# Kernel optimization log

Hardware: AMD Instinct MI355X
Metric: run time of the kernel (lower is better)

The kernel has to match this reference:

```python
import math
import jax, jax.numpy as jnp
import numpy as np


def get_slopes(n):
    def pow2(n):
        start = 2.0 ** (-(2.0 ** (-(math.log2(n) - 3))))
        return [start * (start ** i) for i in range(n)]
    if math.log2(n).is_integer():
        return pow2(n)
    c = 2 ** math.floor(math.log2(n))
    return pow2(c) + get_slopes(2 * c)[0::2][: n - c]


def setup_inputs() -> dict:
    key = jax.random.key(0)
    B, T, C = 2, 2048, 1024
    ks = jax.random.split(key, 9)
    std = 0.02
    n_layers = 12
    inp = {
        "x": jax.random.normal(ks[0], (B, T, C), dtype=jnp.float32),
        # weights stored as [in, out] (transpose of torch Linear.weight)
        "Wq": std * jax.random.normal(ks[1], (C, C), dtype=jnp.float32),
        "bq": jnp.zeros((C,), dtype=jnp.float32),
        "Wk": std * jax.random.normal(ks[2], (C, C), dtype=jnp.float32),
        "bk": jnp.zeros((C,), dtype=jnp.float32),
        "Wv": std * jax.random.normal(ks[3], (C, C), dtype=jnp.float32),
        "bv": jnp.zeros((C,), dtype=jnp.float32),
        # fc_resid gets std 0.02/sqrt(2*num_layers)
        "Wo": (std / math.sqrt(2 * n_layers)) * jax.random.normal(ks[4], (C, C), dtype=jnp.float32),
        "bo": jnp.zeros((C,), dtype=jnp.float32),
        "n_head": 16,
    }
    return inp


def reference(x, Wq, bq, Wk, bk, Wv, bv, Wo, bo, n_head):
    B, T, C = x.shape
    hd = C // n_head
    # QKV projections, split heads: [B, nh, T, hd]
    def proj(W, b):
        return (x @ W + b).reshape(B, T, n_head, hd).transpose(0, 2, 1, 3)
    q, k, v = proj(Wq, bq), proj(Wk, bk), proj(Wv, bv)

    # ALiBi bias: bias[h, i, j] = -slope_h * (i - j) for j <= i, -inf above diag
    slopes = jnp.asarray(get_slopes(n_head), dtype=x.dtype)  # [nh]
    idx = jnp.arange(T)
    dist = (idx[:, None] - idx[None, :]).astype(x.dtype)  # [T, T], i - j
    bias = -slopes[:, None, None] * dist  # [nh, T, T]
    causal = idx[:, None] >= idx[None, :]
    bias = jnp.where(causal[None], bias, jnp.asarray(-jnp.inf, dtype=x.dtype))

    scale = 1.0 / math.sqrt(hd)
    scores = jnp.einsum("bnqh,bnkh->bnqk", q, k) * scale + bias[None]
    att = jax.nn.softmax(scores, axis=-1)
    y = jnp.einsum("bnqk,bnkh->bnqh", att, v)  # [B, nh, T, hd]
    y = y.transpose(0, 2, 1, 3).reshape(B, T, C)
    return y @ Wo + bo
```

## Files before the change

kernel.cpp:

```cpp
#include <hip/hip_runtime.h>


typedef unsigned short u16;
typedef unsigned int u32;
typedef __attribute__((ext_vector_type(8))) short bf16x8;
typedef __attribute__((ext_vector_type(4))) float f32x4;
typedef __attribute__((ext_vector_type(4))) unsigned short u16x4;

#define MFMA16x16(A, B, C_) __builtin_amdgcn_mfma_f32_16x16x32_bf16((A), (B), (C_), 0, 0, 0)

__device__ __forceinline__ u16 f2bf(float f) {
  u32 x = __builtin_bit_cast(u32, f);
  x += 0x7fff + ((x >> 16) & 1);
  return (u16)(x >> 16);
}

__device__ __forceinline__ void gload_lds16(const u16* g, u16* l) {
  __builtin_amdgcn_global_load_lds(
      (const __attribute__((address_space(1))) void*)g,
      (__attribute__((address_space(3))) void*)l, 16, 0, 0);
}

constexpr int T = 2048, C = 1024, HD = 64;
constexpr int BT = 2 * T;

__device__ __forceinline__ bf16x8 ldsfrag(const u16* lds, int row, int kchunk) {
  return *(const bf16x8*)(lds + row * 64 + (((kchunk) ^ (row & 7)) << 3));
}

__global__ __launch_bounds__(256) void convert_x_kernel(
    const float* __restrict__ xin, u16* __restrict__ xc) {
  int i = (blockIdx.x * 256 + threadIdx.x) * 8;
  const float4 a = *(const float4*)(xin + i);
  const float4 b = *(const float4*)(xin + i + 4);
  uint4 o;
  o.x = (u32)f2bf(a.x) | ((u32)f2bf(a.y) << 16);
  o.y = (u32)f2bf(a.z) | ((u32)f2bf(a.w) << 16);
  o.z = (u32)f2bf(b.x) | ((u32)f2bf(b.y) << 16);
  o.w = (u32)f2bf(b.z) | ((u32)f2bf(b.w) << 16);
  *(uint4*)(xc + i) = o;
}

__global__ __launch_bounds__(256) void transpose4_kernel(
    const float* __restrict__ w0, const float* __restrict__ w1,
    const float* __restrict__ w2, const float* __restrict__ w3,
    u16* __restrict__ wqkvT, u16* __restrict__ woT) {
  __shared__ u16 tile[32][33];
  const int z = blockIdx.z;
  const float* in = (z == 0) ? w0 : (z == 1) ? w1 : (z == 2) ? w2 : w3;
  u16* out = (z < 3) ? (wqkvT + (size_t)z * (1u << 20)) : woT;
  int tx = threadIdx.x, ty = threadIdx.y;
  int x = blockIdx.x * 32 + tx;
#pragma unroll
  for (int i = 0; i < 4; i++) {
    int y = blockIdx.y * 32 + ty + i * 8;
    tile[ty + i * 8][tx] = f2bf(in[y * 1024 + x]);
  }
  __syncthreads();
  int xo = blockIdx.y * 32 + tx;
#pragma unroll
  for (int i = 0; i < 4; i++) {
    int yo = blockIdx.x * 32 + ty + i * 8;
    out[yo * 1024 + xo] = tile[tx][ty + i * 8];
  }
}

__global__ __launch_bounds__(256) void gemm_qkv_kernel(
    const u16* __restrict__ A, const u16* __restrict__ Bt,
    const float* __restrict__ b0, const float* __restrict__ b1,
    const float* __restrict__ b2,
    u16* __restrict__ qout, u16* __restrict__ kout, u16* __restrict__ vtout) {
  constexpr int K = 1024;
  __shared__ __align__(16) u16 As[128 * 64];
  __shared__ __align__(16) u16 Bs[128 * 64];

  const int tid = threadIdx.x;
  const int w = tid >> 6, lane = tid & 63;
  const int l15 = lane & 15, quad = lane >> 4;
  const int m0 = blockIdx.y * 128, n0 = blockIdx.x * 128;
  const int wm = (w >> 1) * 64, wn = (w & 1) * 64;
  const int gsub = (lane & 7) ^ ((lane >> 3) & 7);
  const int rsub = lane >> 3;

  f32x4 acc[4][4] = {};
  const u16* Ag = A + (size_t)m0 * K;
  const u16* Bg = Bt + (size_t)n0 * K;

  for (int k0 = 0; k0 < K; k0 += 64) {
    __syncthreads();
#pragma unroll
    for (int t = 0; t < 4; t++) {
      int rbase = w * 32 + t * 8;
      gload_lds16(Ag + (size_t)(rbase + rsub) * K + k0 + gsub * 8, As + rbase * 64);
      gload_lds16(Bg + (size_t)(rbase + rsub) * K + k0 + gsub * 8, Bs + rbase * 64);
    }
    __syncthreads();
#pragma unroll
    for (int ks = 0; ks < 2; ks++) {
      bf16x8 af[4], bf[4];
#pragma unroll
      for (int mi = 0; mi < 4; mi++)
        af[mi] = ldsfrag(As, wm + mi * 16 + l15, (ks << 2) | quad);
#pragma unroll
      for (int ni = 0; ni < 4; ni++)
        bf[ni] = ldsfrag(Bs, wn + ni * 16 + l15, (ks << 2) | quad);
#pragma unroll
      for (int mi = 0; mi < 4; mi++)
#pragma unroll
        for (int ni = 0; ni < 4; ni++)
          acc[mi][ni] = MFMA16x16(af[mi], bf[ni], acc[mi][ni]);
    }
  }

  const int sel = n0 >> 10;
  const int nloc = n0 & 1023;
  if (sel < 2) {
    u16* D = (sel == 0) ? qout : kout;
    const float* bias = (sel == 0) ? b0 : b1;
#pragma unroll
    for (int mi = 0; mi < 4; mi++)
#pragma unroll
      for (int ni = 0; ni < 4; ni++) {
        int rb = m0 + wm + mi * 16 + quad * 4;
        int col = nloc + wn + ni * 16 + l15;
        float bb = bias[col];
#pragma unroll
        for (int r = 0; r < 4; r++)
          D[(size_t)(rb + r) * 1024 + col] = f2bf(acc[mi][ni][r] + bb);
      }
  } else {
#pragma unroll
    for (int mi = 0; mi < 4; mi++)
#pragma unroll
      for (int ni = 0; ni < 4; ni++) {
        int rb = m0 + wm + mi * 16 + quad * 4;
        int c = nloc + wn + ni * 16 + l15;
        float bb = b2[c];
        u16x4 pk;
#pragma unroll
        for (int r = 0; r < 4; r++) pk[r] = f2bf(acc[mi][ni][r] + bb);
        *(u16x4*)(vtout + (size_t)c * 4096 + rb) = pk;
      }
  }
}

__global__ __launch_bounds__(256) void gemm_out_kernel(
    const u16* __restrict__ A, const u16* __restrict__ Bt,
    const float* __restrict__ bias, float* __restrict__ fout) {
  constexpr int K = 1024;
  __shared__ __align__(16) u16 As[128 * 64];
  __shared__ __align__(16) u16 Bs[64 * 64];

  const int tid = threadIdx.x;
  const int w = tid >> 6, lane = tid & 63;
  const int l15 = lane & 15, quad = lane >> 4;
  const int m0 = blockIdx.y * 128, n0 = blockIdx.x * 64;
  const int wm = (w >> 1) * 64, wn = (w & 1) * 32;
  const int gsub = (lane & 7) ^ ((lane >> 3) & 7);
  const int rsub = lane >> 3;

  f32x4 acc[4][2] = {};
  const u16* Ag = A + (size_t)m0 * K;
  const u16* Bg = Bt + (size_t)n0 * K;

  for (int k0 = 0; k0 < K; k0 += 64) {
    __syncthreads();
#pragma unroll
    for (int t = 0; t < 4; t++) {
      int rbase = w * 32 + t * 8;
      gload_lds16(Ag + (size_t)(rbase + rsub) * K + k0 + gsub * 8, As + rbase * 64);
    }
#pragma unroll
    for (int t = 0; t < 2; t++) {
      int rbase = w * 16 + t * 8;
      gload_lds16(Bg + (size_t)(rbase + rsub) * K + k0 + gsub * 8, Bs + rbase * 64);
    }
    __syncthreads();
#pragma unroll
    for (int ks = 0; ks < 2; ks++) {
      bf16x8 af[4], bf[2];
#pragma unroll
      for (int mi = 0; mi < 4; mi++)
        af[mi] = ldsfrag(As, wm + mi * 16 + l15, (ks << 2) | quad);
#pragma unroll
      for (int ni = 0; ni < 2; ni++)
        bf[ni] = ldsfrag(Bs, wn + ni * 16 + l15, (ks << 2) | quad);
#pragma unroll
      for (int mi = 0; mi < 4; mi++)
#pragma unroll
        for (int ni = 0; ni < 2; ni++)
          acc[mi][ni] = MFMA16x16(af[mi], bf[ni], acc[mi][ni]);
    }
  }

#pragma unroll
  for (int mi = 0; mi < 4; mi++)
#pragma unroll
    for (int ni = 0; ni < 2; ni++) {
      int rb = m0 + wm + mi * 16 + quad * 4;
      int col = n0 + wn + ni * 16 + l15;
      float bb = bias[col];
#pragma unroll
      for (int r = 0; r < 4; r++)
        fout[(size_t)(rb + r) * 1024 + col] = acc[mi][ni][r] + bb;
    }
}

__global__ __launch_bounds__(512, 4) void attn_kernel(
    const u16* __restrict__ qbuf, const u16* __restrict__ kbuf,
    const u16* __restrict__ vtbuf, u16* __restrict__ ybuf) {
  __shared__ __align__(16) u16 Qs[64 * 64];
  __shared__ __align__(16) u16 KVs[4][64 * 64];
  __shared__ __align__(16) u16 Ps[8][16 * 64];

  const int tid = threadIdx.x;
  const int w = tid >> 6, lane = tid & 63;
  const int wq = w & 3, g = w >> 2;
  const int l15 = lane & 15, quad = lane >> 4;
  const int bh = blockIdx.y, b = bh >> 4, h = bh & 15;
  const float slope = exp2f(-0.5f * (float)(h + 1));
  const float slope128 = slope * 128.f;
  const int gsub = (lane & 7) ^ ((lane >> 3) & 7);
  const int rsub = lane >> 3;

  const u16* kbase0 = kbuf + (size_t)b * T * C + h * HD;
  const u16* vtbase0 = vtbuf + (size_t)h * HD * BT + (size_t)b * T;
  u16* Pw = Ps[w];
  const int st = w >> 1;
  const int skind = st & 1;
  const int sjt = st >> 1;
  const int srb = (w & 1) * 32;

#pragma unroll 1
  for (int half = 0; half < 2; half++) {
    const int qt = half == 0 ? (31 - (int)blockIdx.x) : (int)blockIdx.x;

    __syncthreads();
    const u16* qb = qbuf + (size_t)(b * T + qt * 64) * C + h * HD;
    gload_lds16(qb + (size_t)(w * 8 + rsub) * C + gsub * 8, Qs + (w * 8) * 64);
    __syncthreads();
    bf16x8 aq0 = ldsfrag(Qs, wq * 16 + l15, quad);
    bf16x8 aq1 = ldsfrag(Qs, wq * 16 + l15, 4 + quad);

    f32x4 o[4] = {};
    float lsum[4] = {0.f, 0.f, 0.f, 0.f};
    float br[4][4];
    const int ig0 = qt * 64 + wq * 16 + quad * 4;
#pragma unroll
    for (int ni = 0; ni < 4; ni++)
#pragma unroll
      for (int r = 0; r < 4; r++)
        br[ni][r] = slope * (float)(g * 64 + ni * 16 + l15 - ig0 - r);

    const int iters = (qt + 2) >> 1;
#pragma unroll 1
    for (int it = 0; it < iters; it++) {
      __syncthreads();
      {
        int jtv = 2 * it + sjt;
        int jtr = jtv > qt ? qt : jtv;
        const u16* base = skind ? (vtbase0 + jtr * 64)
                                : (kbase0 + (size_t)jtr * 64 * C);
        const int stride = skind ? BT : C;
        u16* dst = KVs[skind * 2 + sjt] + srb * 64;
#pragma unroll
        for (int c2 = 0; c2 < 4; c2++)
          gload_lds16(base + (size_t)(srb + c2 * 8 + rsub) * stride + gsub * 8,
                      dst + c2 * 8 * 64);
      }
      __syncthreads();

      const int jtv = 2 * it + g;
      const u16* Kw = KVs[g];
      const u16* Vw = KVs[2 + g];

      f32x4 s[4];
#pragma unroll
      for (int ni = 0; ni < 4; ni++) {
        bf16x8 kf0 = ldsfrag(Kw, ni * 16 + l15, quad);
        bf16x8 kf1 = ldsfrag(Kw, ni * 16 + l15, 4 + quad);
        f32x4 z = {0.f, 0.f, 0.f, 0.f};
        z = MFMA16x16(aq0, kf0, z);
        z = MFMA16x16(aq1, kf1, z);
        s[ni] = z;
      }

      const bool edge = (jtv >= qt);
#pragma unroll
      for (int ni = 0; ni < 4; ni++)
#pragma unroll
        for (int r = 0; r < 4; r++) {
          float p = __expf(fmaf(s[ni][r], 0.125f, br[ni][r]));
          if (edge && (jtv * 64 + ni * 16 + l15) > (ig0 + r)) p = 0.f;
          lsum[r] += p;
          int prow = quad * 4 + r, pcol = ni * 16 + l15;
          Pw[prow * 64 + (((pcol >> 3) ^ (prow & 7)) << 3) + (pcol & 7)] = f2bf(p);
          br[ni][r] += slope128;
        }

      bf16x8 pa0 = ldsfrag(Pw, l15, quad);
      bf16x8 pa1 = ldsfrag(Pw, l15, 4 + quad);
#pragma unroll
      for (int ni = 0; ni < 4; ni++) {
        bf16x8 vf0 = ldsfrag(Vw, ni * 16 + l15, quad);
        bf16x8 vf1 = ldsfrag(Vw, ni * 16 + l15, 4 + quad);
        o[ni] = MFMA16x16(pa0, vf0, o[ni]);
        o[ni] = MFMA16x16(pa1, vf1, o[ni]);
      }
    }

    __syncthreads();
    float* sc = (float*)KVs;
    float* Osc = sc + wq * 1024;
    float* Lsc = sc + 4096 + wq * 256;
    if (g == 1) {
#pragma unroll
      for (int ni = 0; ni < 4; ni++)
#pragma unroll
        for (int r = 0; r < 4; r++)
          Osc[(quad * 4 + r) * 64 + ni * 16 + l15] = o[ni][r];
#pragma unroll
      for (int r = 0; r < 4; r++)
        Lsc[(quad * 4 + r) * 16 + l15] = lsum[r];
    }
    __syncthreads();
    if (g == 0) {
#pragma unroll
      for (int ni = 0; ni < 4; ni++)
#pragma unroll
        for (int r = 0; r < 4; r++)
          o[ni][r] += Osc[(quad * 4 + r) * 64 + ni * 16 + l15];
#pragma unroll
      for (int r = 0; r < 4; r++) {
        float l = lsum[r] + Lsc[(quad * 4 + r) * 16 + l15];
        l += __shfl_xor(l, 1);
        l += __shfl_xor(l, 2);
        l += __shfl_xor(l, 4);
        l += __shfl_xor(l, 8);
        float inv = 1.f / l;
        int row_g = b * T + qt * 64 + wq * 16 + quad * 4 + r;
        u16* yrow = ybuf + (size_t)row_g * C + h * HD;
#pragma unroll
        for (int ni = 0; ni < 4; ni++)
          yrow[ni * 16 + l15] = f2bf(o[ni][r] * inv);
      }
    }
  }
}

extern "C" void kernel_launch(void* const* d_in, const int* in_sizes, int n_in,
                              void* d_out, int out_size, void* d_ws, size_t ws_size,
                              hipStream_t stream) {
  (void)in_sizes; (void)n_in; (void)out_size; (void)ws_size;
  const float* x  = (const float*)d_in[0];
  const float* Wq = (const float*)d_in[1];
  const float* bq = (const float*)d_in[2];
  const float* Wk = (const float*)d_in[3];
  const float* bk = (const float*)d_in[4];
  const float* Wv = (const float*)d_in[5];
  const float* bv = (const float*)d_in[6];
  const float* Wo = (const float*)d_in[7];
  const float* bo = (const float*)d_in[8];

  u16* ws = (u16*)d_ws;
  constexpr size_t M1 = 1u << 20;
  u16* wqkvT = ws;
  u16* woT   = ws + 3 * M1;
  u16* xc    = ws + 4 * M1;
  u16* qbuf  = ws + 8 * M1;
  u16* vtbuf = ws + 12 * M1;
  u16* kbuf  = (u16*)d_out;
  u16* ybuf  = qbuf;

  convert_x_kernel<<<2048, 256, 0, stream>>>(x, xc);
  transpose4_kernel<<<dim3(32, 32, 4), dim3(32, 8), 0, stream>>>(Wq, Wk, Wv, Wo, wqkvT, woT);
  gemm_qkv_kernel<<<dim3(24, 32), 256, 0, stream>>>(
      xc, wqkvT, bq, bk, bv, qbuf, kbuf, vtbuf);
  attn_kernel<<<dim3(16, 32), 512, 0, stream>>>(qbuf, kbuf, vtbuf, ybuf);
  gemm_out_kernel<<<dim3(16, 32), 256, 0, stream>>>(ybuf, woT, bo, (float*)d_out);
}
```

Before: 199.3 us.

## Double attention query tile to 128 rows per block for K/V reuse

Each attention block now handles a 128-row query tile: every wave computes two 16-row sub-blocks, so each K/V tile loaded into LDS serves twice as many query rows. The grid shrinks to 8x32 blocks, launch bounds drop to 2 blocks per CU, and shared memory is merged into one aliased buffer, with the P scratch overlapping the Q region. This reduces global K/V traffic and sync overhead per unit of work. In exchange it uses more registers and runs fewer blocks, which can hurt occupancy and load balance across CUs.

Measured after the change: 208.8 us. 4.8% more time.

```diff
diff --git a/kernel.cpp b/kernel.cpp
--- a/kernel.cpp
+++ b/kernel.cpp
@@ -206,12 +206,10 @@
     }
 }
 
-__global__ __launch_bounds__(512, 4) void attn_kernel(
+__global__ __launch_bounds__(512, 2) void attn_kernel(
     const u16* __restrict__ qbuf, const u16* __restrict__ kbuf,
     const u16* __restrict__ vtbuf, u16* __restrict__ ybuf) {
-  __shared__ __align__(16) u16 Qs[64 * 64];
-  __shared__ __align__(16) u16 KVs[4][64 * 64];
-  __shared__ __align__(16) u16 Ps[8][16 * 64];
+  __shared__ __align__(16) u16 SMEM[24576];
 
   const int tid = threadIdx.x;
   const int w = tid >> 6, lane = tid & 63;
@@ -220,49 +218,61 @@
   const int bh = blockIdx.y, b = bh >> 4, h = bh & 15;
   const float slope = exp2f(-0.5f * (float)(h + 1));
   const float slope128 = slope * 128.f;
+  const float s16 = slope * 16.f;
   const int gsub = (lane & 7) ^ ((lane >> 3) & 7);
   const int rsub = lane >> 3;
 
+  u16* Qs = SMEM;
+  u16* KVs = SMEM + 8192;
+  u16* Pw = SMEM + w * 1024;
+
   const u16* kbase0 = kbuf + (size_t)b * T * C + h * HD;
   const u16* vtbase0 = vtbuf + (size_t)h * HD * BT + (size_t)b * T;
-  u16* Pw = Ps[w];
+
   const int st = w >> 1;
-  const int skind = st & 1;
-  const int sjt = st >> 1;
+  const int skind = st >> 1;
+  const int sjt = st & 1;
   const int srb = (w & 1) * 32;
 
 #pragma unroll 1
   for (int half = 0; half < 2; half++) {
-    const int qt = half == 0 ? (31 - (int)blockIdx.x) : (int)blockIdx.x;
-
-    __syncthreads();
-    const u16* qb = qbuf + (size_t)(b * T + qt * 64) * C + h * HD;
-    gload_lds16(qb + (size_t)(w * 8 + rsub) * C + gsub * 8, Qs + (w * 8) * 64);
-    __syncthreads();
-    bf16x8 aq0 = ldsfrag(Qs, wq * 16 + l15, quad);
-    bf16x8 aq1 = ldsfrag(Qs, wq * 16 + l15, 4 + quad);
-
-    f32x4 o[4] = {};
-    float lsum[4] = {0.f, 0.f, 0.f, 0.f};
+    const int qt = half == 0 ? (15 - (int)blockIdx.x) : (int)blockIdx.x;
+    const int qrow_g = b * T + qt * 128;
+
+    __syncthreads();
+    const u16* qb = qbuf + (size_t)qrow_g * C + h * HD;
+#pragma unroll
+    for (int t = 0; t < 2; t++)
+      gload_lds16(qb + (size_t)(w * 16 + t * 8 + rsub) * C + gsub * 8,
+                  Qs + (w * 16 + t * 8) * 64);
+    __syncthreads();
+    bf16x8 aq[2][2];
+#pragma unroll
+    for (int sb = 0; sb < 2; sb++) {
+      aq[sb][0] = ldsfrag(Qs, wq * 32 + sb * 16 + l15, quad);
+      aq[sb][1] = ldsfrag(Qs, wq * 32 + sb * 16 + l15, 4 + quad);
+    }
+
+    f32x4 o[2][4] = {};
+    float lsum[2][4] = {};
+    const int ig00 = qt * 128 + wq * 32;
     float br[4][4];
-    const int ig0 = qt * 64 + wq * 16 + quad * 4;
 #pragma unroll
     for (int ni = 0; ni < 4; ni++)
 #pragma unroll
       for (int r = 0; r < 4; r++)
-        br[ni][r] = slope * (float)(g * 64 + ni * 16 + l15 - ig0 - r);
-
-    const int iters = (qt + 2) >> 1;
+        br[ni][r] = slope * (float)(g * 64 + ni * 16 + l15 - ig00 - quad * 4 - r);
+
+    const int iters = qt + 1;
 #pragma unroll 1
     for (int it = 0; it < iters; it++) {
       __syncthreads();
       {
-        int jtv = 2 * it + sjt;
-        int jtr = jtv > qt ? qt : jtv;
-        const u16* base = skind ? (vtbase0 + jtr * 64)
-                                : (kbase0 + (size_t)jtr * 64 * C);
+        int jt = 2 * it + sjt;
+        const u16* base = skind ? (vtbase0 + jt * 64)
+                                : (kbase0 + (size_t)jt * 64 * C);
         const int stride = skind ? BT : C;
-        u16* dst = KVs[skind * 2 + sjt] + srb * 64;
+        u16* dst = KVs + st * 4096 + srb * 64;
 #pragma unroll
         for (int c2 = 0; c2 < 4; c2++)
           gload_lds16(base + (size_t)(srb + c2 * 8 + rsub) * stride + gsub * 8,
@@ -271,79 +281,89 @@
       __syncthreads();
 
       const int jtv = 2 * it + g;
-      const u16* Kw = KVs[g];
-      const u16* Vw = KVs[2 + g];
-
-      f32x4 s[4];
+      const u16* Kw = KVs + g * 4096;
+      const u16* Vw = KVs + (2 + g) * 4096;
+
+      f32x4 s[2][4];
 #pragma unroll
       for (int ni = 0; ni < 4; ni++) {
         bf16x8 kf0 = ldsfrag(Kw, ni * 16 + l15, quad);
         bf16x8 kf1 = ldsfrag(Kw, ni * 16 + l15, 4 + quad);
-        f32x4 z = {0.f, 0.f, 0.f, 0.f};
-        z = MFMA16x16(aq0, kf0, z);
-        z = MFMA16x16(aq1, kf1, z);
-        s[ni] = z;
-      }
-
-      const bool edge = (jtv >= qt);
+#pragma unroll
+        for (int sb = 0; sb < 2; sb++) {
+          f32x4 z = {0.f, 0.f, 0.f, 0.f};
+          z = MFMA16x16(aq[sb][0], kf0, z);
+          z = MFMA16x16(aq[sb][1], kf1, z);
+          s[sb][ni] = z;
+        }
+      }
+
+#pragma unroll
+      for (int sb = 0; sb < 2; sb++) {
+        const float boff = sb ? s16 : 0.f;
+        const int igs = ig00 + sb * 16 + quad * 4;
+        const bool edge = (jtv * 64 + 63) > (ig00 + sb * 16);
+#pragma unroll
+        for (int ni = 0; ni < 4; ni++)
+#pragma unroll
+          for (int r = 0; r < 4; r++) {
+            float p = __expf(fmaf(s[sb][ni][r], 0.125f, br[ni][r] - boff));
+            if (edge && (jtv * 64 + ni * 16 + l15) > (igs + r)) p = 0.f;
+            lsum[sb][r] += p;
+            int prow = quad * 4 + r, pcol = ni * 16 + l15;
+            Pw[prow * 64 + (((pcol >> 3) ^ (prow & 7)) << 3) + (pcol & 7)] = f2bf(p);
+          }
+        bf16x8 pa0 = ldsfrag(Pw, l15, quad);
+        bf16x8 pa1 = ldsfrag(Pw, l15, 4 + quad);
+#pragma unroll
+        for (int ni = 0; ni < 4; ni++) {
+          bf16x8 vf0 = ldsfrag(Vw, ni * 16 + l15, quad);
+          bf16x8 vf1 = ldsfrag(Vw, ni * 16 + l15, 4 + quad);
+          o[sb][ni] = MFMA16x16(pa0, vf0, o[sb][ni]);
+          o[sb][ni] = MFMA16x16(pa1, vf1, o[sb][ni]);
+        }
+      }
 #pragma unroll
       for (int ni = 0; ni < 4; ni++)
 #pragma unroll
+        for (int r = 0; r < 4; r++) br[ni][r] += slope128;
+    }
+
+    __syncthreads();
+    float* Osc = (float*)(SMEM + 8192);
+    float* Lsc = (float*)SMEM;
+    if (g == 1) {
+#pragma unroll
+      for (int sb = 0; sb < 2; sb++) {
+#pragma unroll
+        for (int ni = 0; ni < 4; ni++)
+#pragma unroll
+          for (int r = 0; r < 4; r++)
+            Osc[(wq * 32 + sb * 16 + quad * 4 + r) * 64 + ni * 16 + l15] = o[sb][ni][r];
+#pragma unroll
+        for (int r = 0; r < 4; r++)
+          Lsc[(wq * 32 + sb * 16 + quad * 4 + r) * 16 + l15] = lsum[sb][r];
+      }
+    }
+    __syncthreads();
+    if (g == 0) {
+#pragma unroll
+      for (int sb = 0; sb < 2; sb++)
+#pragma unroll
         for (int r = 0; r < 4; r++) {
-          float p = __expf(fmaf(s[ni][r], 0.125f, br[ni][r]));
-          if (edge && (jtv * 64 + ni * 16 + l15) > (ig0 + r)) p = 0.f;
-          lsum[r] += p;
-          int prow = quad * 4 + r, pcol = ni * 16 + l15;
-          Pw[prow * 64 + (((pcol >> 3) ^ (prow & 7)) << 3) + (pcol & 7)] = f2bf(p);
-          br[ni][r] += slope128;
+          int lrow = wq * 32 + sb * 16 + quad * 4 + r;
+          float l = lsum[sb][r] + Lsc[lrow * 16 + l15];
+          l += __shfl_xor(l, 1);
+          l += __shfl_xor(l, 2);
+          l += __shfl_xor(l, 4);
+          l += __shfl_xor(l, 8);
+          float inv = 1.f / l;
+          u16* yrow = ybuf + (size_t)(qrow_g + lrow) * C + h * HD;
+#pragma unroll
+          for (int ni = 0; ni < 4; ni++)
+            yrow[ni * 16 + l15] =
+                f2bf((o[sb][ni][r] + Osc[lrow * 64 + ni * 16 + l15]) * inv);
         }
-
-      bf16x8 pa0 = ldsfrag(Pw, l15, quad);
-      bf16x8 pa1 = ldsfrag(Pw, l15, 4 + quad);
-#pragma unroll
-      for (int ni = 0; ni < 4; ni++) {
-        bf16x8 vf0 = ldsfrag(Vw, ni * 16 + l15, quad);
-        bf16x8 vf1 = ldsfrag(Vw, ni * 16 + l15, 4 + quad);
-        o[ni] = MFMA16x16(pa0, vf0, o[ni]);
-        o[ni] = MFMA16x16(pa1, vf1, o[ni]);
-      }
-    }
-
-    __syncthreads();
-    float* sc = (float*)KVs;
-    float* Osc = sc + wq * 1024;
-    float* Lsc = sc + 4096 + wq * 256;
-    if (g == 1) {
-#pragma unroll
-      for (int ni = 0; ni < 4; ni++)
-#pragma unroll
-        for (int r = 0; r < 4; r++)
-          Osc[(quad * 4 + r) * 64 + ni * 16 + l15] = o[ni][r];
-#pragma unroll
-      for (int r = 0; r < 4; r++)
-        Lsc[(quad * 4 + r) * 16 + l15] = lsum[r];
-    }
-    __syncthreads();
-    if (g == 0) {
-#pragma unroll
-      for (int ni = 0; ni < 4; ni++)
-#pragma unroll
-        for (int r = 0; r < 4; r++)
-          o[ni][r] += Osc[(quad * 4 + r) * 64 + ni * 16 + l15];
-#pragma unroll
-      for (int r = 0; r < 4; r++) {
-        float l = lsum[r] + Lsc[(quad * 4 + r) * 16 + l15];
-        l += __shfl_xor(l, 1);
-        l += __shfl_xor(l, 2);
-        l += __shfl_xor(l, 4);
-        l += __shfl_xor(l, 8);
-        float inv = 1.f / l;
-        int row_g = b * T + qt * 64 + wq * 16 + quad * 4 + r;
-        u16* yrow = ybuf + (size_t)row_g * C + h * HD;
-#pragma unroll
-        for (int ni = 0; ni < 4; ni++)
-          yrow[ni * 16 + l15] = f2bf(o[ni][r] * inv);
-      }
     }
   }
 }
@@ -376,6 +396,6 @@
   transpose4_kernel<<<dim3(32, 32, 4), dim3(32, 8), 0, stream>>>(Wq, Wk, Wv, Wo, wqkvT, woT);
   gemm_qkv_kernel<<<dim3(24, 32), 256, 0, stream>>>(
       xc, wqkvT, bq, bk, bv, qbuf, kbuf, vtbuf);
-  attn_kernel<<<dim3(16, 32), 512, 0, stream>>>(qbuf, kbuf, vtbuf, ybuf);
+  attn_kernel<<<dim3(8, 32), 512, 0, stream>>>(qbuf, kbuf, vtbuf, ybuf);
   gemm_out_kernel<<<dim3(16, 32), 256, 0, stream>>>(ybuf, woT, bo, (float*)d_out);
 }
```

## Split attention blocks per query tile, transpose score MFMA, merge prep kernels

Applied to the files above, without the earlier changes.

The attention kernel no longer processes two paired query tiles per block. It launches one block per query tile with a larger grid, higher occupancy bounds, and LDS overlapped into a single aliased buffer. The score MFMA operands are swapped so each lane holds a query column, which lets P be written as packed 8-byte stores and reduces the row-sum reduction to two shuffles. The x conversion and weight transpose kernels are merged into one launch. The work per block is now imbalanced under the causal mask, and the longest blocks are scheduled first to offset this.

Result: slower. 242.6 us (+21.7%).

```diff
diff --git a/kernel.cpp b/kernel.cpp
--- a/kernel.cpp
+++ b/kernel.cpp
@@ -28,28 +28,30 @@
   return *(const bf16x8*)(lds + row * 64 + (((kchunk) ^ (row & 7)) << 3));
 }
 
-__global__ __launch_bounds__(256) void convert_x_kernel(
-    const float* __restrict__ xin, u16* __restrict__ xc) {
-  int i = (blockIdx.x * 256 + threadIdx.x) * 8;
-  const float4 a = *(const float4*)(xin + i);
-  const float4 b = *(const float4*)(xin + i + 4);
-  uint4 o;
-  o.x = (u32)f2bf(a.x) | ((u32)f2bf(a.y) << 16);
-  o.y = (u32)f2bf(a.z) | ((u32)f2bf(a.w) << 16);
-  o.z = (u32)f2bf(b.x) | ((u32)f2bf(b.y) << 16);
-  o.w = (u32)f2bf(b.z) | ((u32)f2bf(b.w) << 16);
-  *(uint4*)(xc + i) = o;
-}
-
-__global__ __launch_bounds__(256) void transpose4_kernel(
-    const float* __restrict__ w0, const float* __restrict__ w1,
-    const float* __restrict__ w2, const float* __restrict__ w3,
-    u16* __restrict__ wqkvT, u16* __restrict__ woT) {
+__global__ __launch_bounds__(256) void prep_kernel(
+    const float* __restrict__ xin, const float* __restrict__ w0,
+    const float* __restrict__ w1, const float* __restrict__ w2,
+    const float* __restrict__ w3, u16* __restrict__ wqkvT,
+    u16* __restrict__ woT, u16* __restrict__ xc) {
+  const int z = blockIdx.z;
+  const int tid = threadIdx.x;
+  if (z >= 4) {
+    int fb = (z - 4) * 1024 + blockIdx.y * 32 + blockIdx.x;
+    int i = (fb * 256 + tid) * 8;
+    const float4 a = *(const float4*)(xin + i);
+    const float4 b = *(const float4*)(xin + i + 4);
+    uint4 o;
+    o.x = (u32)f2bf(a.x) | ((u32)f2bf(a.y) << 16);
+    o.y = (u32)f2bf(a.z) | ((u32)f2bf(a.w) << 16);
+    o.z = (u32)f2bf(b.x) | ((u32)f2bf(b.y) << 16);
+    o.w = (u32)f2bf(b.z) | ((u32)f2bf(b.w) << 16);
+    *(uint4*)(xc + i) = o;
+    return;
+  }
   __shared__ u16 tile[32][33];
-  const int z = blockIdx.z;
   const float* in = (z == 0) ? w0 : (z == 1) ? w1 : (z == 2) ? w2 : w3;
   u16* out = (z < 3) ? (wqkvT + (size_t)z * (1u << 20)) : woT;
-  int tx = threadIdx.x, ty = threadIdx.y;
+  int tx = tid & 31, ty = tid >> 5;
   int x = blockIdx.x * 32 + tx;
 #pragma unroll
   for (int i = 0; i < 4; i++) {
@@ -206,144 +208,141 @@
     }
 }
 
-__global__ __launch_bounds__(512, 4) void attn_kernel(
+__global__ __launch_bounds__(512, 6) void attn_kernel(
     const u16* __restrict__ qbuf, const u16* __restrict__ kbuf,
     const u16* __restrict__ vtbuf, u16* __restrict__ ybuf) {
-  __shared__ __align__(16) u16 Qs[64 * 64];
-  __shared__ __align__(16) u16 KVs[4][64 * 64];
-  __shared__ __align__(16) u16 Ps[8][16 * 64];
+  __shared__ __align__(16) u16 SMEM[24576];
 
   const int tid = threadIdx.x;
   const int w = tid >> 6, lane = tid & 63;
   const int wq = w & 3, g = w >> 2;
   const int l15 = lane & 15, quad = lane >> 4;
   const int bh = blockIdx.y, b = bh >> 4, h = bh & 15;
+  const int qt = 31 - (int)blockIdx.x;
   const float slope = exp2f(-0.5f * (float)(h + 1));
   const float slope128 = slope * 128.f;
   const int gsub = (lane & 7) ^ ((lane >> 3) & 7);
   const int rsub = lane >> 3;
 
+  u16* Qs = SMEM;
+  u16* KVs = SMEM + 4096;
+  u16* Pw = (w < 4) ? (SMEM + w * 1024)
+                    : (SMEM + 20480 + (w - 4) * 1024);
+
   const u16* kbase0 = kbuf + (size_t)b * T * C + h * HD;
   const u16* vtbase0 = vtbuf + (size_t)h * HD * BT + (size_t)b * T;
-  u16* Pw = Ps[w];
+
   const int st = w >> 1;
   const int skind = st & 1;
   const int sjt = st >> 1;
   const int srb = (w & 1) * 32;
 
+  const u16* qb = qbuf + (size_t)(b * T + qt * 64) * C + h * HD;
+  gload_lds16(qb + (size_t)(w * 8 + rsub) * C + gsub * 8, Qs + (w * 8) * 64);
+  __syncthreads();
+  bf16x8 aq0 = ldsfrag(Qs, wq * 16 + l15, quad);
+  bf16x8 aq1 = ldsfrag(Qs, wq * 16 + l15, 4 + quad);
+
+  f32x4 o[4] = {};
+  float lsum = 0.f;
+  const int ig0 = qt * 64 + wq * 16;
+  float br[4][4];
+#pragma unroll
+  for (int ni = 0; ni < 4; ni++)
+#pragma unroll
+    for (int r = 0; r < 4; r++)
+      br[ni][r] = slope * (float)(g * 64 + ni * 16 + quad * 4 + r - ig0 - l15);
+
+  const int iters = (qt + 2) >> 1;
 #pragma unroll 1
-  for (int half = 0; half < 2; half++) {
-    const int qt = half == 0 ? (31 - (int)blockIdx.x) : (int)blockIdx.x;
-
-    __syncthreads();
-    const u16* qb = qbuf + (size_t)(b * T + qt * 64) * C + h * HD;
-    gload_lds16(qb + (size_t)(w * 8 + rsub) * C + gsub * 8, Qs + (w * 8) * 64);
-    __syncthreads();
-    bf16x8 aq0 = ldsfrag(Qs, wq * 16 + l15, quad);
-    bf16x8 aq1 = ldsfrag(Qs, wq * 16 + l15, 4 + quad);
-
-    f32x4 o[4] = {};
-    float lsum[4] = {0.f, 0.f, 0.f, 0.f};
-    float br[4][4];
-    const int ig0 = qt * 64 + wq * 16 + quad * 4;
+  for (int it = 0; it < iters; it++) {
+    __syncthreads();
+    {
+      int jtv = 2 * it + sjt;
+      int jtr = jtv > qt ? qt : jtv;
+      const u16* base = skind ? (vtbase0 + jtr * 64)
+                              : (kbase0 + (size_t)jtr * 64 * C);
+      const int stride = skind ? BT : C;
+      u16* dst = KVs + (skind * 2 + sjt) * 4096 + srb * 64;
+#pragma unroll
+      for (int c2 = 0; c2 < 4; c2++)
+        gload_lds16(base + (size_t)(srb + c2 * 8 + rsub) * stride + gsub * 8,
+                    dst + c2 * 8 * 64);
+    }
+    __syncthreads();
+
+    const int jtv = 2 * it + g;
+    const u16* Kw = KVs + g * 4096;
+    const u16* Vw = KVs + (2 + g) * 4096;
+
+    f32x4 s[4];
+#pragma unroll
+    for (int ni = 0; ni < 4; ni++) {
+      bf16x8 kf0 = ldsfrag(Kw, ni * 16 + l15, quad);
+      bf16x8 kf1 = ldsfrag(Kw, ni * 16 + l15, 4 + quad);
+      f32x4 z = {0.f, 0.f, 0.f, 0.f};
+      z = MFMA16x16(kf0, aq0, z);
+      z = MFMA16x16(kf1, aq1, z);
+      s[ni] = z;
+    }
+
+    const bool edge = (jtv >= qt);
+    const int iabs = ig0 + l15;
+#pragma unroll
+    for (int ni = 0; ni < 4; ni++) {
+      float pr[4];
+#pragma unroll
+      for (int r = 0; r < 4; r++) {
+        float p = __expf(fmaf(s[ni][r], 0.125f, br[ni][r]));
+        if (edge && (jtv * 64 + ni * 16 + quad * 4 + r) > iabs) p = 0.f;
+        lsum += p;
+        pr[r] = p;
+        br[ni][r] += slope128;
+      }
+      u32 lo = (u32)f2bf(pr[0]) | ((u32)f2bf(pr[1]) << 16);
+      u32 hi = (u32)f2bf(pr[2]) | ((u32)f2bf(pr[3]) << 16);
+      int chunk = (ni * 2 + (quad >> 1)) ^ (l15 & 7);
+      uint2 pk = {lo, hi};
+      *(uint2*)(Pw + l15 * 64 + chunk * 8 + (quad & 1) * 4) = pk;
+    }
+
+    bf16x8 pa0 = ldsfrag(Pw, l15, quad);
+    bf16x8 pa1 = ldsfrag(Pw, l15, 4 + quad);
+#pragma unroll
+    for (int ni = 0; ni < 4; ni++) {
+      bf16x8 vf0 = ldsfrag(Vw, ni * 16 + l15, quad);
+      bf16x8 vf1 = ldsfrag(Vw, ni * 16 + l15, 4 + quad);
+      o[ni] = MFMA16x16(pa0, vf0, o[ni]);
+      o[ni] = MFMA16x16(pa1, vf1, o[ni]);
+    }
+  }
+
+  __syncthreads();
+  float* Osc = (float*)(SMEM + 4096);
+  float* Lsc = (float*)(SMEM + 20480);
+  if (g == 1) {
 #pragma unroll
     for (int ni = 0; ni < 4; ni++)
 #pragma unroll
       for (int r = 0; r < 4; r++)
-        br[ni][r] = slope * (float)(g * 64 + ni * 16 + l15 - ig0 - r);
-
-    const int iters = (qt + 2) >> 1;
-#pragma unroll 1
-    for (int it = 0; it < iters; it++) {
-      __syncthreads();
-      {
-        int jtv = 2 * it + sjt;
-        int jtr = jtv > qt ? qt : jtv;
-        const u16* base = skind ? (vtbase0 + jtr * 64)
-                                : (kbase0 + (size_t)jtr * 64 * C);
-        const int stride = skind ? BT : C;
-        u16* dst = KVs[skind * 2 + sjt] + srb * 64;
-#pragma unroll
-        for (int c2 = 0; c2 < 4; c2++)
-          gload_lds16(base + (size_t)(srb + c2 * 8 + rsub) * stride + gsub * 8,
-                      dst + c2 * 8 * 64);
-      }
-      __syncthreads();
-
-      const int jtv = 2 * it + g;
-      const u16* Kw = KVs[g];
-      const u16* Vw = KVs[2 + g];
-
-      f32x4 s[4];
-#pragma unroll
-      for (int ni = 0; ni < 4; ni++) {
-        bf16x8 kf0 = ldsfrag(Kw, ni * 16 + l15, quad);
-        bf16x8 kf1 = ldsfrag(Kw, ni * 16 + l15, 4 + quad);
-        f32x4 z = {0.f, 0.f, 0.f, 0.f};
-        z = MFMA16x16(aq0, kf0, z);
-        z = MFMA16x16(aq1, kf1, z);
-        s[ni] = z;
-      }
-
-      const bool edge = (jtv >= qt);
+        Osc[(wq * 16 + quad * 4 + r) * 64 + ni * 16 + l15] = o[ni][r];
+    Lsc[wq * 64 + quad * 16 + l15] = lsum;
+  }
+  __syncthreads();
+  if (g == 0) {
+    float l = lsum + Lsc[wq * 64 + quad * 16 + l15];
+    l += __shfl_xor(l, 16);
+    l += __shfl_xor(l, 32);
+    float inv = 1.f / l;
+#pragma unroll
+    for (int r = 0; r < 4; r++) {
+      float invr = __shfl(inv, (lane & 48) | (quad * 4 + r), 64);
+      int row_g = b * T + ig0 + quad * 4 + r;
+      u16* yrow = ybuf + (size_t)row_g * C + h * HD;
 #pragma unroll
       for (int ni = 0; ni < 4; ni++)
-#pragma unroll
-        for (int r = 0; r < 4; r++) {
-          float p = __expf(fmaf(s[ni][r], 0.125f, br[ni][r]));
-          if (edge && (jtv * 64 + ni * 16 + l15) > (ig0 + r)) p = 0.f;
-          lsum[r] += p;
-          int prow = quad * 4 + r, pcol = ni * 16 + l15;
-          Pw[prow * 64 + (((pcol >> 3) ^ (prow & 7)) << 3) + (pcol & 7)] = f2bf(p);
-          br[ni][r] += slope128;
-        }
-
-      bf16x8 pa0 = ldsfrag(Pw, l15, quad);
-      bf16x8 pa1 = ldsfrag(Pw, l15, 4 + quad);
-#pragma unroll
-      for (int ni = 0; ni < 4; ni++) {
-        bf16x8 vf0 = ldsfrag(Vw, ni * 16 + l15, quad);
-        bf16x8 vf1 = ldsfrag(Vw, ni * 16 + l15, 4 + quad);
-        o[ni] = MFMA16x16(pa0, vf0, o[ni]);
-        o[ni] = MFMA16x16(pa1, vf1, o[ni]);
-      }
-    }
-
-    __syncthreads();
-    float* sc = (float*)KVs;
-    float* Osc = sc + wq * 1024;
-    float* Lsc = sc + 4096 + wq * 256;
-    if (g == 1) {
-#pragma unroll
-      for (int ni = 0; ni < 4; ni++)
-#pragma unroll
-        for (int r = 0; r < 4; r++)
-          Osc[(quad * 4 + r) * 64 + ni * 16 + l15] = o[ni][r];
-#pragma unroll
-      for (int r = 0; r < 4; r++)
-        Lsc[(quad * 4 + r) * 16 + l15] = lsum[r];
-    }
-    __syncthreads();
-    if (g == 0) {
-#pragma unroll
-      for (int ni = 0; ni < 4; ni++)
-#pragma unroll
-        for (int r = 0; r < 4; r++)
-          o[ni][r] += Osc[(quad * 4 + r) * 64 + ni * 16 + l15];
-#pragma unroll
-      for (int r = 0; r < 4; r++) {
-        float l = lsum[r] + Lsc[(quad * 4 + r) * 16 + l15];
-        l += __shfl_xor(l, 1);
-        l += __shfl_xor(l, 2);
-        l += __shfl_xor(l, 4);
-        l += __shfl_xor(l, 8);
-        float inv = 1.f / l;
-        int row_g = b * T + qt * 64 + wq * 16 + quad * 4 + r;
-        u16* yrow = ybuf + (size_t)row_g * C + h * HD;
-#pragma unroll
-        for (int ni = 0; ni < 4; ni++)
-          yrow[ni * 16 + l15] = f2bf(o[ni][r] * inv);
-      }
+        yrow[ni * 16 + l15] =
+            f2bf((o[ni][r] + Osc[(wq * 16 + quad * 4 + r) * 64 + ni * 16 + l15]) * invr);
     }
   }
 }
@@ -372,10 +371,9 @@
   u16* kbuf  = (u16*)d_out;
   u16* ybuf  = qbuf;
 
-  convert_x_kernel<<<2048, 256, 0, stream>>>(x, xc);
-  transpose4_kernel<<<dim3(32, 32, 4), dim3(32, 8), 0, stream>>>(Wq, Wk, Wv, Wo, wqkvT, woT);
+  prep_kernel<<<dim3(32, 32, 6), 256, 0, stream>>>(x, Wq, Wk, Wv, Wo, wqkvT, woT, xc);
   gemm_qkv_kernel<<<dim3(24, 32), 256, 0, stream>>>(
       xc, wqkvT, bq, bk, bv, qbuf, kbuf, vtbuf);
-  attn_kernel<<<dim3(16, 32), 512, 0, stream>>>(qbuf, kbuf, vtbuf, ybuf);
+  attn_kernel<<<dim3(32, 32), 512, 0, stream>>>(qbuf, kbuf, vtbuf, ybuf);
   gemm_out_kernel<<<dim3(16, 32), 256, 0, stream>>>(ybuf, woT, bo, (float*)d_out);
 }
```
